# Kernel tuning notes

Measured on AMD Instinct MI355X. Metric: run time of the kernel, lower is better.

The kernel has to match this reference:

```python
import jax, jax.numpy as jnp
import numpy as np

NUM_ATT_HEADS = 8
NUM_LAYERS = 12
NUM_HEADS = NUM_ATT_HEADS * NUM_LAYERS  # 96
EDGE_HID = 256 // NUM_ATT_HEADS  # 32
NUM_EDGES = 1536
NUM_SPATIAL = 512
NUM_EDGE_DIS = 128
MULTI_HOP = 5


def setup_inputs() -> dict:
    key = jax.random.key(0)
    ks = jax.random.split(key, 8)
    B, N = 16, 128
    attn_bias = jax.random.normal(ks[0], (B, N + 1, N + 1), dtype=jnp.float32)
    spatial_pos = jax.random.randint(ks[1], (B, N, N), 0, NUM_SPATIAL)
    node_attr = jax.random.normal(ks[2], (B, N, 8), dtype=jnp.float32)
    edge_input = jax.random.randint(ks[3], (B, N, N, MULTI_HOP, 3), 0, NUM_EDGES)
    # learned parameters (embedding tables); padding_idx=0 rows zeroed
    edge_enc_w = jax.random.normal(ks[4], (NUM_EDGES + 1, EDGE_HID), dtype=jnp.float32) * 0.02
    edge_enc_w = edge_enc_w.at[0].set(0.0)
    edge_dis_w = jax.random.normal(ks[5], (NUM_EDGE_DIS * EDGE_HID * NUM_HEADS, 1), dtype=jnp.float32) * 0.02
    spatial_enc_w = jax.random.normal(ks[6], (NUM_SPATIAL + 10, NUM_HEADS), dtype=jnp.float32) * 0.02
    spatial_enc_w = spatial_enc_w.at[0].set(0.0)
    virt_w = jax.random.normal(ks[7], (1, NUM_HEADS), dtype=jnp.float32) * 0.02
    return {"attn_bias": attn_bias, "spatial_pos": spatial_pos, "node_attr": node_attr,
            "edge_input": edge_input, "edge_enc_w": edge_enc_w, "edge_dis_w": edge_dis_w,
            "spatial_enc_w": spatial_enc_w, "virt_w": virt_w}


def reference(attn_bias, spatial_pos, node_attr, edge_input, edge_enc_w, edge_dis_w, spatial_enc_w, virt_w):
    B, N = node_attr.shape[:2]
    H = NUM_HEADS
    g = jnp.broadcast_to(attn_bias[:, None], (B, H, N + 1, N + 1))
    # spatial position bias: [B,N,N,H] -> [B,H,N,N]
    spb = spatial_enc_w[spatial_pos].transpose(0, 3, 1, 2)
    g = g.at[:, :, 1:, 1:].add(spb)
    # graph-token virtual distance
    t = virt_w.reshape(1, H, 1)
    g = g.at[:, :, 1:, 0].add(t)
    g = g.at[:, :, 0, :].add(t)
    # hop-count normalizer
    sp = jnp.where(spatial_pos == 0, 1, spatial_pos)
    sp = jnp.where(sp > 1, sp - 1, sp)
    sp = jnp.clip(sp, 0, MULTI_HOP)
    # edge encoding: gather + mean over edge-feature axis -> [B,N,N,D,EDGE_HID]
    ei = edge_enc_w[edge_input[:, :, :, :MULTI_HOP, :]].mean(-2)
    max_dist = ei.shape[-2]
    # per-distance projection EDGE_HID -> H (the torch bmm over flattened dims)
    W = edge_dis_w.reshape(-1, EDGE_HID, H)[:max_dist]  # [D,EDGE_HID,H]
    eh = jnp.einsum('bnmdk,dkh->bnmdh', ei, W)  # [B,N,N,D,H]
    eb = eh.sum(-2) / sp.astype(ei.dtype)[..., None]  # [B,N,N,H]
    g = g.at[:, :, 1:, 1:].add(eb.transpose(0, 3, 1, 2))
    g = g + attn_bias[:, None]
    g = g.reshape(B, NUM_LAYERS, NUM_ATT_HEADS, N + 1, N + 1).transpose(1, 0, 2, 3, 4)
    return g
```

## Files before the change

kernel.cpp:

```cpp
#include <hip/hip_runtime.h>
#include <hip/hip_bf16.h>

#define NH 96
#define NE 1537
#define ND 5
#define NN 128
#define NB 16
#define NP1 129
#define OUT_PLANE (NP1 * NP1)

__device__ __forceinline__ float bflo(unsigned u) { return __uint_as_float(u << 16); }
__device__ __forceinline__ float bfhi(unsigned u) { return __uint_as_float(u & 0xffff0000u); }

__global__ __launch_bounds__(256) void k_build_M(
    const float* __restrict__ E, const float* __restrict__ Wd,
    unsigned short* __restrict__ M) {
  int o = blockIdx.x * 256 + threadIdx.x;
  if (o >= ND * NE * NH) return;
  int h = o % NH;
  int r = o / NH;
  int e = r % NE;
  int d = r / NE;
  const float* __restrict__ Er = E + e * 32;
  const float* __restrict__ Wp = Wd + d * 32 * NH + h;
  float acc = 0.f;
#pragma unroll
  for (int k = 0; k < 32; ++k) acc = fmaf(Er[k], Wp[k * NH], acc);
  unsigned u = __float_as_uint(acc);
  unsigned rb = (u + 0x7fffu + ((u >> 16) & 1u)) >> 16;
  M[o] = (unsigned short)rb;
}

__global__ __launch_bounds__(256) void k_interior(
    const float* __restrict__ ab, const int* __restrict__ spos,
    const int* __restrict__ eidx, const float* __restrict__ spw,
    const unsigned short* __restrict__ M, float* __restrict__ out) {
  const int jt = blockIdx.x;
  const int n  = blockIdx.y;
  const int b  = blockIdx.z;
  const int i  = n + 1;
  const int j0 = jt * 64;

  __shared__ int   s_idx[960];
  __shared__ int   s_sp[64];
  __shared__ float s_eb[64][97];

  const int tid = threadIdx.x;
  const int pairbase = (b * NN + n) * NN + j0;
  const int* __restrict__ ebase = eidx + pairbase * 15;
  for (int k = tid; k < 960; k += 256) s_idx[k] = ebase[k];
  if (tid < 64) s_sp[tid] = spos[pairbase + tid];
  __syncthreads();

  const int p  = tid >> 2;
  const int q  = tid & 3;
  const int hq = q * 24;

  float acc[24];
#pragma unroll
  for (int c = 0; c < 24; ++c) acc[c] = 0.f;

  const int* mi = s_idx + p * 15;
#pragma unroll
  for (int g = 0; g < 15; ++g) {
    const int d = g / 3;
    const int e = mi[g];
    const uint4* __restrict__ r = (const uint4*)(M + (d * NE + e) * NH + hq);
    uint4 a0 = r[0], a1 = r[1], a2 = r[2];
    unsigned w[12] = {a0.x, a0.y, a0.z, a0.w, a1.x, a1.y, a1.z, a1.w,
                      a2.x, a2.y, a2.z, a2.w};
#pragma unroll
    for (int c = 0; c < 12; ++c) {
      acc[2 * c]     += bflo(w[c]);
      acc[2 * c + 1] += bfhi(w[c]);
    }
  }

  const int spn = s_sp[p];
  const int spc = min(max(spn - 1, 1), 5);
  const float scale = 1.0f / (3.0f * (float)spc);

  const float4* __restrict__ sr = (const float4*)(spw + spn * NH + hq);
  float4 sv4[6];
#pragma unroll
  for (int c = 0; c < 6; ++c) sv4[c] = sr[c];
  const float* sv = (const float*)sv4;

#pragma unroll
  for (int c = 0; c < 24; ++c) s_eb[p][hq + c] = acc[c] * scale + sv[c];
  __syncthreads();

  const int jl = tid & 63;
  const int hb = tid >> 6;
  const float a2v = 2.0f * ab[(b * NP1 + i) * NP1 + 1 + j0 + jl];
  const int obase = i * NP1 + 1 + j0 + jl;
#pragma unroll
  for (int it = 0; it < 24; ++it) {
    const int h = it * 4 + hb;
    const float v = s_eb[jl][h] + a2v;
    out[((h >> 3) * 128 + b * 8 + (h & 7)) * OUT_PLANE + obase] = v;
  }
}

__global__ __launch_bounds__(512) void k_boundary(
    const float* __restrict__ ab, const float* __restrict__ virt,
    float* __restrict__ out) {
  const int bh = blockIdx.x;
  const int b = bh / NH;
  const int h = bh % NH;
  const float t = virt[h];
  const int tid = threadIdx.x;
  const int base = ((h >> 3) * 128 + b * 8 + (h & 7)) * OUT_PLANE;
  if (tid < NP1) {
    out[base + tid] = 2.f * ab[(b * NP1) * NP1 + tid] + t;
  } else if (tid < NP1 + NN) {
    const int i = tid - 128;
    out[base + i * NP1] = 2.f * ab[(b * NP1 + i) * NP1] + t;
  }
}

extern "C" void kernel_launch(void* const* d_in, const int* in_sizes, int n_in,
                              void* d_out, int out_size, void* d_ws, size_t ws_size,
                              hipStream_t stream) {
  const float* ab   = (const float*)d_in[0];
  const int*   spos = (const int*)d_in[1];
  const int*   eidx = (const int*)d_in[3];
  const float* eenc = (const float*)d_in[4];
  const float* edis = (const float*)d_in[5];
  const float* spw  = (const float*)d_in[6];
  const float* virt = (const float*)d_in[7];
  float* out = (float*)d_out;

  unsigned short* M = (unsigned short*)d_ws;

  const int totM = ND * NE * NH;
  k_build_M<<<(totM + 255) / 256, 256, 0, stream>>>(eenc, edis, M);
  k_interior<<<dim3(2, NN, NB), 256, 0, stream>>>(ab, spos, eidx, spw, M, out);
  k_boundary<<<NB * NH, 512, 0, stream>>>(ab, virt, out);
}
```

Before: 231.8 us.

## Halve interior tile to 32 columns, split heads 8-way, use nontemporal stores

The interior kernel now handles 32 j-columns per block, with 8 threads per pair each gathering 12 heads, and the grid is doubled. Index loads become int4 vectorized, and the scale and spatial-bias add move to the store phase. Output stores become nontemporal, the boundary kernel now uses 256 threads, and launch bounds request 5 blocks per CU. The aim is more parallelism and occupancy and less cache pollution from the large output write, at the cost of narrower 8-byte gathers and shorter 128-byte store runs per head.

```diff
diff --git a/kernel.cpp b/kernel.cpp
--- a/kernel.cpp
+++ b/kernel.cpp
@@ -31,7 +31,7 @@
   M[o] = (unsigned short)rb;
 }
 
-__global__ __launch_bounds__(256) void k_interior(
+__global__ __launch_bounds__(256, 5) void k_interior(
     const float* __restrict__ ab, const int* __restrict__ spos,
     const int* __restrict__ eidx, const float* __restrict__ spw,
     const unsigned short* __restrict__ M, float* __restrict__ out) {
@@ -39,70 +39,70 @@
   const int n  = blockIdx.y;
   const int b  = blockIdx.z;
   const int i  = n + 1;
-  const int j0 = jt * 64;
+  const int j0 = jt * 32;
 
-  __shared__ int   s_idx[960];
-  __shared__ int   s_sp[64];
-  __shared__ float s_eb[64][97];
+  __shared__ int   s_idx[480];
+  __shared__ int   s_sp[32];
+  __shared__ float s_eb[32][97];
 
   const int tid = threadIdx.x;
   const int pairbase = (b * NN + n) * NN + j0;
-  const int* __restrict__ ebase = eidx + pairbase * 15;
-  for (int k = tid; k < 960; k += 256) s_idx[k] = ebase[k];
-  if (tid < 64) s_sp[tid] = spos[pairbase + tid];
+  if (tid < 120) {
+    ((int4*)s_idx)[tid] = ((const int4*)(eidx + (long)pairbase * 15))[tid];
+  }
+  if (tid >= 128 && tid < 160) s_sp[tid - 128] = spos[pairbase + (tid - 128)];
   __syncthreads();
 
-  const int p  = tid >> 2;
-  const int q  = tid & 3;
-  const int hq = q * 24;
+  const int p  = tid >> 3;
+  const int q  = tid & 7;
+  const int hq = q * 12;
 
-  float acc[24];
+  float acc[12];
 #pragma unroll
-  for (int c = 0; c < 24; ++c) acc[c] = 0.f;
+  for (int c = 0; c < 12; ++c) acc[c] = 0.f;
 
   const int* mi = s_idx + p * 15;
 #pragma unroll
   for (int g = 0; g < 15; ++g) {
     const int d = g / 3;
     const int e = mi[g];
-    const uint4* __restrict__ r = (const uint4*)(M + (d * NE + e) * NH + hq);
-    uint4 a0 = r[0], a1 = r[1], a2 = r[2];
-    unsigned w[12] = {a0.x, a0.y, a0.z, a0.w, a1.x, a1.y, a1.z, a1.w,
-                      a2.x, a2.y, a2.z, a2.w};
-#pragma unroll
-    for (int c = 0; c < 12; ++c) {
-      acc[2 * c]     += bflo(w[c]);
-      acc[2 * c + 1] += bfhi(w[c]);
-    }
+    const uint2* __restrict__ r = (const uint2*)(M + (d * NE + e) * NH + hq);
+    uint2 w0 = r[0], w1 = r[1], w2 = r[2];
+    acc[0]  += bflo(w0.x); acc[1]  += bfhi(w0.x);
+    acc[2]  += bflo(w0.y); acc[3]  += bfhi(w0.y);
+    acc[4]  += bflo(w1.x); acc[5]  += bfhi(w1.x);
+    acc[6]  += bflo(w1.y); acc[7]  += bfhi(w1.y);
+    acc[8]  += bflo(w2.x); acc[9]  += bfhi(w2.x);
+    acc[10] += bflo(w2.y); acc[11] += bfhi(w2.y);
   }
 
-  const int spn = s_sp[p];
+#pragma unroll
+  for (int c = 0; c < 12; ++c) s_eb[p][hq + c] = acc[c];
+  __syncthreads();
+
+  const int jl = tid & 31;
+  const int hb = tid >> 5;
+  const int spn = s_sp[jl];
   const int spc = min(max(spn - 1, 1), 5);
   const float scale = 1.0f / (3.0f * (float)spc);
+  const float a2v = 2.0f * ab[(b * NP1 + i) * NP1 + 1 + j0 + jl];
+  const int obase = i * NP1 + 1 + j0 + jl;
 
-  const float4* __restrict__ sr = (const float4*)(spw + spn * NH + hq);
-  float4 sv4[6];
-#pragma unroll
-  for (int c = 0; c < 6; ++c) sv4[c] = sr[c];
-  const float* sv = (const float*)sv4;
+  const float4* __restrict__ sr = (const float4*)(spw + spn * NH + hb * 12);
+  float4 s0 = sr[0], s1 = sr[1], s2 = sr[2];
+  float sv[12] = {s0.x, s0.y, s0.z, s0.w, s1.x, s1.y, s1.z, s1.w,
+                  s2.x, s2.y, s2.z, s2.w};
 
 #pragma unroll
-  for (int c = 0; c < 24; ++c) s_eb[p][hq + c] = acc[c] * scale + sv[c];
-  __syncthreads();
-
-  const int jl = tid & 63;
-  const int hb = tid >> 6;
-  const float a2v = 2.0f * ab[(b * NP1 + i) * NP1 + 1 + j0 + jl];
-  const int obase = i * NP1 + 1 + j0 + jl;
-#pragma unroll
-  for (int it = 0; it < 24; ++it) {
-    const int h = it * 4 + hb;
-    const float v = s_eb[jl][h] + a2v;
-    out[((h >> 3) * 128 + b * 8 + (h & 7)) * OUT_PLANE + obase] = v;
+  for (int c = 0; c < 12; ++c) {
+    const int h = hb * 12 + c;
+    const float v = s_eb[jl][h] * scale + sv[c] + a2v;
+    __builtin_nontemporal_store(
+        v, &out[((h >> 3) * 128 + b * 8 + (h & 7)) * OUT_PLANE + obase]);
   }
 }
 
-__global__ __launch_bounds__(512) void k_boundary(
+__global__ __launch_bounds__(256) void k_boundary(
     const float* __restrict__ ab, const float* __restrict__ virt,
     float* __restrict__ out) {
   const int bh = blockIdx.x;
@@ -112,10 +112,13 @@
   const int tid = threadIdx.x;
   const int base = ((h >> 3) * 128 + b * 8 + (h & 7)) * OUT_PLANE;
   if (tid < NP1) {
-    out[base + tid] = 2.f * ab[(b * NP1) * NP1 + tid] + t;
-  } else if (tid < NP1 + NN) {
-    const int i = tid - 128;
-    out[base + i * NP1] = 2.f * ab[(b * NP1 + i) * NP1] + t;
+    __builtin_nontemporal_store(2.f * ab[(b * NP1) * NP1 + tid] + t,
+                                &out[base + tid]);
+  }
+  if (tid < NN) {
+    const int i = tid + 1;
+    __builtin_nontemporal_store(2.f * ab[(b * NP1 + i) * NP1] + t,
+                                &out[base + i * NP1]);
   }
 }
 
@@ -135,6 +138,6 @@
 
   const int totM = ND * NE * NH;
   k_build_M<<<(totM + 255) / 256, 256, 0, stream>>>(eenc, edis, M);
-  k_interior<<<dim3(2, NN, NB), 256, 0, stream>>>(ab, spos, eidx, spw, M, out);
-  k_boundary<<<NB * NH, 512, 0, stream>>>(ab, virt, out);
+  k_interior<<<dim3(4, NN, NB), 256, 0, stream>>>(ab, spos, eidx, spw, M, out);
+  k_boundary<<<NB * NH, 256, 0, stream>>>(ab, virt, out);
 }
```

After: 328.7 us. 1.42x slower.
